# Kernel optimization log

Measured on AMD Instinct MI355X. Metric: run time of the kernel, lower is better.

The kernel has to match this reference:

```python
import jax, jax.numpy as jnp
import numpy as np

N, E, H, NODE_IN, EDGE_DIM, L = 10000, 400000, 128, 6, 3, 4
LN_EPS = 1e-5


def _lin_init(key, fan_in, fan_out):
    return jax.random.normal(key, (fan_in, fan_out), dtype=jnp.float32) / np.sqrt(fan_in)


def setup_inputs() -> dict:
    key = jax.random.key(0)
    ks = jax.random.split(key, 24)
    x = jax.random.normal(ks[0], (N, NODE_IN), dtype=jnp.float32)
    edge_index = jax.random.randint(ks[1], (2, E), 0, N, dtype=jnp.int64)
    edge_attr = jax.random.normal(ks[2], (E, EDGE_DIM), dtype=jnp.float32)
    # encoder
    enc_w1 = _lin_init(ks[3], NODE_IN, H); enc_b1 = jnp.zeros((H,), jnp.float32)
    enc_w2 = _lin_init(ks[4], H, H); enc_b2 = jnp.zeros((H,), jnp.float32)
    # per-layer stacked params [L, ...]
    msg_w1 = jax.vmap(lambda k: _lin_init(k, 2 * H + EDGE_DIM, H))(jax.random.split(ks[5], L))
    msg_b1 = jnp.zeros((L, H), jnp.float32)
    msg_w2 = jax.vmap(lambda k: _lin_init(k, H, H))(jax.random.split(ks[6], L))
    msg_b2 = jnp.zeros((L, H), jnp.float32)
    upd_w1 = jax.vmap(lambda k: _lin_init(k, 2 * H, H))(jax.random.split(ks[7], L))
    upd_b1 = jnp.zeros((L, H), jnp.float32)
    upd_w2 = jax.vmap(lambda k: _lin_init(k, H, H))(jax.random.split(ks[8], L))
    upd_b2 = jnp.zeros((L, H), jnp.float32)
    ln_g = jnp.ones((L, H), jnp.float32)
    ln_b = jnp.zeros((L, H), jnp.float32)
    # decoder
    dec_w1 = _lin_init(ks[9], H, H); dec_b1 = jnp.zeros((H,), jnp.float32)
    dec_w2 = _lin_init(ks[10], H, 1); dec_b2 = jnp.zeros((1,), jnp.float32)
    return dict(x=x, edge_index=edge_index, edge_attr=edge_attr,
                enc_w1=enc_w1, enc_b1=enc_b1, enc_w2=enc_w2, enc_b2=enc_b2,
                msg_w1=msg_w1, msg_b1=msg_b1, msg_w2=msg_w2, msg_b2=msg_b2,
                upd_w1=upd_w1, upd_b1=upd_b1, upd_w2=upd_w2, upd_b2=upd_b2,
                ln_g=ln_g, ln_b=ln_b,
                dec_w1=dec_w1, dec_b1=dec_b1, dec_w2=dec_w2, dec_b2=dec_b2)


def _layernorm(h, g, b):
    mu = jnp.mean(h, axis=-1, keepdims=True)
    var = jnp.mean(jnp.square(h - mu), axis=-1, keepdims=True)
    return (h - mu) * jax.lax.rsqrt(var + LN_EPS) * g + b


def reference(x, edge_index, edge_attr,
              enc_w1, enc_b1, enc_w2, enc_b2,
              msg_w1, msg_b1, msg_w2, msg_b2,
              upd_w1, upd_b1, upd_w2, upd_b2,
              ln_g, ln_b,
              dec_w1, dec_b1, dec_w2, dec_b2):
    src, tgt = edge_index[0], edge_index[1]  # PyG default flow: message from x_j=src to x_i=tgt
    # in-degree counts for mean aggregation (zero-degree nodes -> 0 output, like scatter_mean)
    counts = jax.ops.segment_sum(jnp.ones((E,), jnp.float32), tgt, num_segments=N)
    inv_counts = (1.0 / jnp.maximum(counts, 1.0))[:, None]
    # encoder
    h = jax.nn.relu(x @ enc_w1 + enc_b1) @ enc_w2 + enc_b2  # [N, H]
    for l in range(L):
        x_i = h[tgt]  # [E, H] target features
        x_j = h[src]  # [E, H] source features
        m_in = jnp.concatenate([x_i, x_j, edge_attr], axis=-1)  # [E, 2H+edge_dim]
        m = jax.nn.relu(m_in @ msg_w1[l] + msg_b1[l]) @ msg_w2[l] + msg_b2[l]  # [E, H]
        agg = jax.ops.segment_sum(m, tgt, num_segments=N) * inv_counts  # [N, H] mean aggregate
        u_in = jnp.concatenate([h, agg], axis=-1)  # [N, 2H]
        u = jax.nn.relu(u_in @ upd_w1[l] + upd_b1[l]) @ upd_w2[l] + upd_b2[l]
        h = _layernorm(u + h, ln_g[l], ln_b[l])  # residual (in==out channels)
    # decoder
    return jax.nn.relu(h @ dec_w1 + dec_b1) @ dec_w2 + dec_b2  # [N, 1]
```

## Files before the change

kernel.cpp:

```cpp
#include <hip/hip_runtime.h>

#define NN 10000
#define NE 400000
#define HD 128
#define NIN 6
#define EDIM 3
#define NL 4
#define CAP 96
#define LN_EPS 1e-5f

typedef unsigned short u16;
using short8 = __attribute__((ext_vector_type(8))) short;
using f32x4 = __attribute__((ext_vector_type(4))) float;

__device__ __forceinline__ u16 f2bf(float x) {
    unsigned u = __float_as_uint(x);
    return (u16)((u + 0x7fff + ((u >> 16) & 1)) >> 16);
}
__device__ __forceinline__ float bf2f(u16 h) { return __uint_as_float(((unsigned)h) << 16); }
__device__ __forceinline__ void split2(float x, u16& hi, u16& lo) {
    hi = f2bf(x);
    lo = f2bf(x - bf2f(hi));
}
#define MFMA(a, b, c) __builtin_amdgcn_mfma_f32_16x16x32_bf16((a), (b), (c), 0, 0, 0)


__global__ __launch_bounds__(256) void k_prepfrag(
    const float* __restrict__ msg_w2, const float* __restrict__ msg_b2, const float* __restrict__ upd_w1,
    const float* __restrict__ upd_w2, const float* __restrict__ msg_w1, const float* __restrict__ dec_w1,
    const float* __restrict__ enc_w2, float* __restrict__ c2, int* __restrict__ cnt,
    u16* __restrict__ fG1, u16* __restrict__ fG2, u16* __restrict__ fPQ,
    u16* __restrict__ fDec, u16* __restrict__ fEnc) {
    int idx = blockIdx.x * 256 + threadIdx.x;
    if (idx < 65536) {
        int l = idx >> 14, rem = idx & 16383, i = rem >> 7, jj = rem & 127;
        const float* U1b = upd_w1 + (size_t)l * 2 * HD * HD + (size_t)HD * HD;
        const float* W2 = msg_w2 + (size_t)l * HD * HD + (size_t)i * HD;
        float acc = 0.f;
        for (int t = 0; t < HD; ++t) acc += W2[t] * U1b[(size_t)t * HD + jj];
        int ct = jj >> 4;
        int ks = 4 + (i >> 5);
        int lane = (((i & 31) >> 3) << 4) | (jj & 15);
        int j = i & 7;
        int g = (l << 12) | (ct << 9) | (ks << 6) | lane;
        fG1[(size_t)g * 8 + j] = f2bf(acc);
    } else if (idx < 66048) {
        int r = idx - 65536;
        int l = r >> 7, jj = r & 127;
        const float* U1b = upd_w1 + (size_t)l * 2 * HD * HD + (size_t)HD * HD;
        const float* b2 = msg_b2 + l * HD;
        float acc = 0.f;
        for (int t = 0; t < HD; ++t) acc += b2[t] * U1b[(size_t)t * HD + jj];
        c2[r] = acc;
    } else if (idx < 76048) {
        cnt[idx - 66048] = 0;
    } else if (idx < 84240) {
        int gl = idx - 76048;
        int l = gl >> 11, rem = gl & 2047;
        int ct = rem >> 8, ks = (rem >> 6) & 3, lane = rem & 63;
        int n = ct * 16 + (lane & 15), kb = ks * 32 + ((lane >> 4) << 3);
        int g = (l << 12) | (ct << 9) | (ks << 6) | lane;
        u16* dst = fG1 + (size_t)g * 8;
        const float* U = upd_w1 + (size_t)l * 256 * 128;
#pragma unroll
        for (int j = 0; j < 8; ++j) dst[j] = f2bf(U[(size_t)(kb + j) * 128 + n]);
    } else if (idx < 92432) {
        int gg = idx - 84240;
        int l = gg >> 11, r = gg & 2047;
        int ct = r >> 8, ks = (r >> 6) & 3, lane = r & 63;
        int n = ct * 16 + (lane & 15), kb = ks * 32 + ((lane >> 4) << 3);
        u16* dst = fG2 + (size_t)gg * 8;
        const float* W = upd_w2 + (size_t)l * 128 * 128;
#pragma unroll
        for (int j = 0; j < 8; ++j) dst[j] = f2bf(W[(size_t)(kb + j) * 128 + n]);
    } else if (idx < 108816) {
        int gg = idx - 92432;
        int li = gg >> 12, r = gg & 4095;
        int ct = r >> 8, ks = (r >> 6) & 3, lane = r & 63;
        int n = ct * 16 + (lane & 15), kb = ks * 32 + ((lane >> 4) << 3);
        u16* dst = fPQ + (size_t)gg * 8;
        const float* W = msg_w1 + (size_t)li * (2 * HD + EDIM) * HD;
#pragma unroll
        for (int j = 0; j < 8; ++j) {
            int k = kb + j;
            float v = (n < 128) ? W[(size_t)k * 128 + n] : W[(size_t)(128 + k) * 128 + (n - 128)];
            dst[j] = f2bf(v);
        }
    } else if (idx < 110864) {
        int r = idx - 108816;
        int ct = r >> 8, ks = (r >> 6) & 3, lane = r & 63;
        int n = ct * 16 + (lane & 15), kb = ks * 32 + ((lane >> 4) << 3);
        u16* dst = fDec + (size_t)r * 8;
#pragma unroll
        for (int j = 0; j < 8; ++j) dst[j] = f2bf(dec_w1[(size_t)(kb + j) * 128 + n]);
    } else if (idx < 112912) {
        int r = idx - 110864;
        int ct = r >> 8, ks = (r >> 6) & 3, lane = r & 63;
        int n = ct * 16 + (lane & 15), kb = ks * 32 + ((lane >> 4) << 3);
        u16* dst = fEnc + (size_t)r * 8;
#pragma unroll
        for (int j = 0; j < 8; ++j) dst[j] = f2bf(enc_w2[(size_t)(kb + j) * 128 + n]);
    }
}


__global__ __launch_bounds__(512) void k_scatenc(
    const int* __restrict__ srcp, const int* __restrict__ tgtp, const float* __restrict__ eattr,
    int* __restrict__ cnt, float4* __restrict__ sea,
    const float* __restrict__ x, const float* __restrict__ ew1, const float* __restrict__ eb1,
    const u16* __restrict__ fEnc, const float* __restrict__ eb2, const u16* __restrict__ fPQ0,
    const float* __restrict__ mb1, u16* __restrict__ h_hi, u16* __restrict__ h_lo,
    float* __restrict__ PQf, u16* __restrict__ Qb) {
    __shared__ u16 tHi[2048], tLo[2048];
    if (blockIdx.x >= 625) {
        int e = (blockIdx.x - 625) * 512 + threadIdx.x;
        if (e < NE) {
            int t = tgtp[e];
            int pos = atomicAdd(&cnt[t], 1);
            if (pos < CAP) {
                sea[t * CAP + pos] = make_float4(eattr[e * 3], eattr[e * 3 + 1], eattr[e * 3 + 2],
                                                 __uint_as_float((unsigned)srcp[e]));
            }
        }
        return;
    }
    int tid = threadIdx.x, w = tid >> 6, lane = tid & 63, q = lane >> 4, c = lane & 15;
    int band = blockIdx.x * 16;
    {
        int col = w * 16 + c;
        float wv[NIN];
#pragma unroll
        for (int k = 0; k < NIN; ++k) wv[k] = ew1[k * HD + col];
        float ebv = eb1[col];
#pragma unroll
        for (int reg = 0; reg < 4; ++reg) {
            int row = band + q * 4 + reg;
            float t = ebv;
#pragma unroll
            for (int k = 0; k < NIN; ++k) t += x[(size_t)row * NIN + k] * wv[k];
            t = fmaxf(t, 0.f);
            u16 hi, lo;
            split2(t, hi, lo);
            int r16 = q * 4 + reg;
            int a = r16 * 128 + (((col >> 3) ^ r16) << 3) + (col & 7);
            tHi[a] = hi;
            tLo[a] = lo;
        }
    }
    __syncthreads();
    short8 aH[4], aL[4];
#pragma unroll
    for (int ks = 0; ks < 4; ++ks) {
        int a = c * 128 + (((ks * 4 + q) ^ c) << 3);
        aH[ks] = *(const short8*)&tHi[a];
        aL[ks] = *(const short8*)&tLo[a];
    }
    f32x4 acc = {0, 0, 0, 0};
    {
        const u16* fb = fEnc + (size_t)w * 4 * 512 + lane * 8;
#pragma unroll
        for (int ks = 0; ks < 4; ++ks) {
            short8 b = *(const short8*)(fb + ks * 512);
            acc = MFMA(aH[ks], b, acc);
            acc = MFMA(aL[ks], b, acc);
        }
    }
    __syncthreads();
    {
        int col = w * 16 + c;
        float ebv = eb2[col];
#pragma unroll
        for (int reg = 0; reg < 4; ++reg) {
            int r16 = q * 4 + reg, row = band + r16;
            float hval = acc[reg] + ebv;
            u16 hi, lo;
            split2(hval, hi, lo);
            h_hi[(size_t)row * HD + col] = hi;
            h_lo[(size_t)row * HD + col] = lo;
            int a = r16 * 128 + (((col >> 3) ^ r16) << 3) + (col & 7);
            tHi[a] = hi;
            tLo[a] = lo;
        }
    }
    __syncthreads();
#pragma unroll
    for (int ks = 0; ks < 4; ++ks) {
        int a = c * 128 + (((ks * 4 + q) ^ c) << 3);
        aH[ks] = *(const short8*)&tHi[a];
        aL[ks] = *(const short8*)&tLo[a];
    }
#pragma unroll
    for (int i = 0; i < 2; ++i) {
        int ctg = w * 2 + i;
        const u16* fb = fPQ0 + (size_t)ctg * 4 * 512 + lane * 8;
        f32x4 a3 = {0, 0, 0, 0};
#pragma unroll
        for (int ks = 0; ks < 4; ++ks) {
            short8 b = *(const short8*)(fb + ks * 512);
            a3 = MFMA(aH[ks], b, a3);
            a3 = MFMA(aL[ks], b, a3);
        }
        int col = ctg * 16 + c;
        if (ctg < 8) {
            float bias = mb1[col];
#pragma unroll
            for (int reg = 0; reg < 4; ++reg)
                PQf[(size_t)(band + q * 4 + reg) * HD + col] = a3[reg] + bias;
        } else {
            int colq = col - 128;
#pragma unroll
            for (int reg = 0; reg < 4; ++reg)
                Qb[(size_t)(band + q * 4 + reg) * HD + colq] = f2bf(a3[reg]);
        }
    }
}


template <bool LAST>
__global__ __launch_bounds__(512) void k_layer(
    const float* __restrict__ PQf_in, const u16* __restrict__ Qb_in,
    const int* __restrict__ cnt, const float4* __restrict__ sea, const float* __restrict__ wc,
    u16* __restrict__ h_hi, u16* __restrict__ h_lo,
    const u16* __restrict__ fG1, const u16* __restrict__ fG2,
    const float* __restrict__ ub1, const float* __restrict__ c2l, const float* __restrict__ ub2,
    const float* __restrict__ g, const float* __restrict__ bb,
    const u16* __restrict__ fPQ, const float* __restrict__ nb1,
    float* __restrict__ PQf_out, u16* __restrict__ Qb_out,
    const u16* __restrict__ fDec, const float* __restrict__ db1, const float* __restrict__ dw2,
    const float* __restrict__ db2, float* __restrict__ out) {
    __shared__ u16 sHi[2048], sLo[2048];
    __shared__ u16 tHi[2048], tLo[2048];
    __shared__ float red[16][8][2];
    int tid = threadIdx.x, w = tid >> 6, lane = tid & 63, q = lane >> 4, c = lane & 15;
    int band = blockIdx.x * 16;
    int j = lane * 2;
    {
        float2 wcr0 = *(const float2*)(wc + j);
        float2 wcr1 = *(const float2*)(wc + HD + j);
        float2 wcr2 = *(const float2*)(wc + 2 * HD + j);
#pragma unroll
        for (int i = 0; i < 2; ++i) {
            int r16 = w * 2 + i;
            int n = __builtin_amdgcn_readfirstlane(band + r16);
            int cn = cnt[n];
            float invn = 1.0f / fmaxf((float)cn, 1.0f);
            int cle = __builtin_amdgcn_readfirstlane(cn < CAP ? cn : CAP);
            float2 p = *(const float2*)(PQf_in + (size_t)n * HD + j);
            float acc0 = 0.f, acc1 = 0.f;
            const float4* bucket = sea + (size_t)n * CAP;
            auto edge1 = [&](float4 A) {
                int sv = (int)__float_as_uint(A.w);
                float c0 = A.x * wcr0.x + A.y * wcr1.x + A.z * wcr2.x;
                float c1 = A.x * wcr0.y + A.y * wcr1.y + A.z * wcr2.y;
                unsigned u = *(const unsigned*)(Qb_in + (size_t)sv * HD + j);
                acc0 += fmaxf(p.x + __uint_as_float(u << 16) + c0, 0.f);
                acc1 += fmaxf(p.y + __uint_as_float(u & 0xffff0000u) + c1, 0.f);
            };
            int e = 0;
            for (; e + 3 < cle; e += 4) {
                float4 A0 = bucket[e], A1 = bucket[e + 1], A2 = bucket[e + 2], A3 = bucket[e + 3];
                edge1(A0);
                edge1(A1);
                edge1(A2);
                edge1(A3);
            }
            for (; e < cle; ++e) edge1(bucket[e]);
            float v0 = acc0 * invn, v1 = acc1 * invn;
            u16 h0, l0, h1, l1;
            split2(v0, h0, l0);
            split2(v1, h1, l1);
            int a = r16 * 128 + (((j >> 3) ^ r16) << 3) + (j & 7);
            *(ushort2*)&sHi[a] = make_ushort2(h0, h1);
            *(ushort2*)&sLo[a] = make_ushort2(l0, l1);
        }
    }
    __syncthreads();
    short8 aH[8], aL[8];
    {
        size_t rb = (size_t)(band + c) * HD + q * 8;
#pragma unroll
        for (int ks = 0; ks < 4; ++ks) {
            aH[ks] = *(const short8*)(h_hi + rb + ks * 32);
            aL[ks] = *(const short8*)(h_lo + rb + ks * 32);
            int a = c * 128 + (((ks * 4 + q) ^ c) << 3);
            aH[4 + ks] = *(const short8*)&sHi[a];
            aL[4 + ks] = *(const short8*)&sLo[a];
        }
    }
    f32x4 acc = {0, 0, 0, 0};
    {
        const u16* fb = fG1 + (size_t)w * 8 * 512 + lane * 8;
#pragma unroll
        for (int ks = 0; ks < 8; ++ks) {
            short8 b = *(const short8*)(fb + ks * 512);
            acc = MFMA(aH[ks], b, acc);
            acc = MFMA(aL[ks], b, acc);
        }
    }
    float alv[4];
#pragma unroll
    for (int reg = 0; reg < 4; ++reg) alv[reg] = (cnt[band + q * 4 + reg] > 0) ? 1.f : 0.f;
    {
        int col = w * 16 + c;
        float u1b = ub1[col], cc = c2l[col];
#pragma unroll
        for (int reg = 0; reg < 4; ++reg) {
            int r16 = q * 4 + reg;
            float t = fmaxf(acc[reg] + u1b + alv[reg] * cc, 0.f);
            u16 hi, lo;
            split2(t, hi, lo);
            int a = r16 * 128 + (((col >> 3) ^ r16) << 3) + (col & 7);
            tHi[a] = hi;
            tLo[a] = lo;
        }
    }
    __syncthreads();
    short8 aH2[4], aL2[4];
#pragma unroll
    for (int ks = 0; ks < 4; ++ks) {
        int a = c * 128 + (((ks * 4 + q) ^ c) << 3);
        aH2[ks] = *(const short8*)&tHi[a];
        aL2[ks] = *(const short8*)&tLo[a];
    }
    f32x4 acc2 = {0, 0, 0, 0};
    {
        const u16* fb = fG2 + (size_t)w * 4 * 512 + lane * 8;
#pragma unroll
        for (int ks = 0; ks < 4; ++ks) {
            short8 b = *(const short8*)(fb + ks * 512);
            acc2 = MFMA(aH2[ks], b, acc2);
            acc2 = MFMA(aL2[ks], b, acc2);
        }
    }
    float vv[4];
    {
        int col = w * 16 + c;
        float u2b = ub2[col];
#pragma unroll
        for (int reg = 0; reg < 4; ++reg) {
            size_t idx = (size_t)(band + q * 4 + reg) * HD + col;
            float hres = bf2f(h_hi[idx]) + bf2f(h_lo[idx]);
            vv[reg] = acc2[reg] + u2b + hres;
        }
    }
#pragma unroll
    for (int reg = 0; reg < 4; ++reg) {
        float s = vv[reg];
        float s2 = vv[reg] * vv[reg];
        for (int m = 1; m < 16; m <<= 1) {
            s += __shfl_xor(s, m);
            s2 += __shfl_xor(s2, m);
        }
        if (c == 0) {
            red[q * 4 + reg][w][0] = s;
            red[q * 4 + reg][w][1] = s2;
        }
    }
    __syncthreads();
    float mu[4], rs[4];
#pragma unroll
    for (int reg = 0; reg < 4; ++reg) {
        int r16 = q * 4 + reg;
        float S1 = 0.f, S2 = 0.f;
#pragma unroll
        for (int ww = 0; ww < 8; ++ww) {
            S1 += red[r16][ww][0];
            S2 += red[r16][ww][1];
        }
        float m = S1 * (1.f / HD);
        float var = S2 * (1.f / HD) - m * m;
        mu[reg] = m;
        rs[reg] = rsqrtf(var + LN_EPS);
    }
    {
        int col = w * 16 + c;
        float gg = g[col], bv = bb[col];
#pragma unroll
        for (int reg = 0; reg < 4; ++reg) {
            int r16 = q * 4 + reg;
            float o = (vv[reg] - mu[reg]) * rs[reg] * gg + bv;
            u16 hi, lo;
            split2(o, hi, lo);
            int a = r16 * 128 + (((col >> 3) ^ r16) << 3) + (col & 7);
            tHi[a] = hi;
            tLo[a] = lo;
            if (!LAST) {
                size_t idx = (size_t)(band + r16) * HD + col;
                h_hi[idx] = hi;
                h_lo[idx] = lo;
            }
        }
    }
    __syncthreads();
    short8 aH3[4], aL3[4];
#pragma unroll
    for (int ks = 0; ks < 4; ++ks) {
        int a = c * 128 + (((ks * 4 + q) ^ c) << 3);
        aH3[ks] = *(const short8*)&tHi[a];
        aL3[ks] = *(const short8*)&tLo[a];
    }
    if (!LAST) {
#pragma unroll
        for (int i = 0; i < 2; ++i) {
            int ctg = w * 2 + i;
            const u16* fb = fPQ + (size_t)ctg * 4 * 512 + lane * 8;
            f32x4 a3 = {0, 0, 0, 0};
#pragma unroll
            for (int ks = 0; ks < 4; ++ks) {
                short8 b = *(const short8*)(fb + ks * 512);
                a3 = MFMA(aH3[ks], b, a3);
                a3 = MFMA(aL3[ks], b, a3);
            }
            int col = ctg * 16 + c;
            if (ctg < 8) {
                float bias = nb1[col];
#pragma unroll
                for (int reg = 0; reg < 4; ++reg)
                    PQf_out[(size_t)(band + q * 4 + reg) * HD + col] = a3[reg] + bias;
            } else {
                int colq = col - 128;
#pragma unroll
                for (int reg = 0; reg < 4; ++reg)
                    Qb_out[(size_t)(band + q * 4 + reg) * HD + colq] = f2bf(a3[reg]);
            }
        }
    } else {
        float part[4];
        {
            const u16* fb = fDec + (size_t)w * 4 * 512 + lane * 8;
            f32x4 a3 = {0, 0, 0, 0};
#pragma unroll
            for (int ks = 0; ks < 4; ++ks) {
                short8 b = *(const short8*)(fb + ks * 512);
                a3 = MFMA(aH3[ks], b, a3);
                a3 = MFMA(aL3[ks], b, a3);
            }
            int col = w * 16 + c;
            float w2v = dw2[col], b1v = db1[col];
#pragma unroll
            for (int reg = 0; reg < 4; ++reg) part[reg] = fmaxf(a3[reg] + b1v, 0.f) * w2v;
        }
#pragma unroll
        for (int reg = 0; reg < 4; ++reg) {
            float s = part[reg];
            for (int m = 1; m < 16; m <<= 1) s += __shfl_xor(s, m);
            if (c == 0) red[q * 4 + reg][w][0] = s;
        }
        __syncthreads();
        if (tid < 16) {
            float s = db2[0];
#pragma unroll
            for (int ww = 0; ww < 8; ++ww) s += red[tid][ww][0];
            out[band + tid] = s;
        }
    }
}


extern "C" void kernel_launch(void* const* d_in, const int* in_sizes, int n_in,
                              void* d_out, int out_size, void* d_ws, size_t ws_size,
                              hipStream_t stream) {
    const float* x = (const float*)d_in[0];
    const int* eidx = (const int*)d_in[1];
    const float* eattr = (const float*)d_in[2];
    const float* enc_w1 = (const float*)d_in[3];
    const float* enc_b1 = (const float*)d_in[4];
    const float* enc_w2 = (const float*)d_in[5];
    const float* enc_b2 = (const float*)d_in[6];
    const float* msg_w1 = (const float*)d_in[7];
    const float* msg_b1 = (const float*)d_in[8];
    const float* msg_w2 = (const float*)d_in[9];
    const float* msg_b2 = (const float*)d_in[10];
    const float* upd_w1 = (const float*)d_in[11];
    const float* upd_b1 = (const float*)d_in[12];
    const float* upd_w2 = (const float*)d_in[13];
    const float* upd_b2 = (const float*)d_in[14];
    const float* ln_g = (const float*)d_in[15];
    const float* ln_b = (const float*)d_in[16];
    const float* dec_w1 = (const float*)d_in[17];
    const float* dec_b1 = (const float*)d_in[18];
    const float* dec_w2 = (const float*)d_in[19];
    const float* dec_b2 = (const float*)d_in[20];
    const int* srcp = eidx;
    const int* tgtp = eidx + NE;

    char* base = (char*)d_ws;
    size_t off = 0;
    auto alloc = [&](size_t bytes) -> void* {
        off = (off + 15) & ~(size_t)15;
        void* p = base + off;
        off += bytes;
        return p;
    };
    float4* sea = (float4*)alloc((size_t)NN * CAP * 16);
    float* PQf0 = (float*)alloc((size_t)NN * HD * 4);
    float* PQf1 = (float*)alloc((size_t)NN * HD * 4);
    u16* Qb0 = (u16*)alloc((size_t)NN * HD * 2);
    u16* Qb1 = (u16*)alloc((size_t)NN * HD * 2);
    u16* h_hi = (u16*)alloc((size_t)NN * HD * 2);
    u16* h_lo = (u16*)alloc((size_t)NN * HD * 2);
    int* cnt = (int*)alloc((size_t)NN * 4);
    float* c2 = (float*)alloc((size_t)NL * HD * 4);
    u16* fG1 = (u16*)alloc((size_t)131072 * 2);
    u16* fG2 = (u16*)alloc((size_t)65536 * 2);
    u16* fPQ = (u16*)alloc((size_t)131072 * 2);
    u16* fDec = (u16*)alloc((size_t)16384 * 2);
    u16* fEnc = (u16*)alloc((size_t)16384 * 2);

    k_prepfrag<<<442, 256, 0, stream>>>(msg_w2, msg_b2, upd_w1, upd_w2, msg_w1, dec_w1, enc_w2,
                                        c2, cnt, fG1, fG2, fPQ, fDec, fEnc);
    k_scatenc<<<625 + (NE + 511) / 512, 512, 0, stream>>>(srcp, tgtp, eattr, cnt, sea,
                                                          x, enc_w1, enc_b1, fEnc, enc_b2, fPQ,
                                                          msg_b1, h_hi, h_lo, PQf0, Qb0);

    float* PQin = PQf0;
    u16* Qin = Qb0;
    float* PQout = PQf1;
    u16* Qout = Qb1;
    for (int l = 0; l < NL; ++l) {
        const float* wc = msg_w1 + (size_t)l * (2 * HD + EDIM) * HD + (size_t)2 * HD * HD;
        if (l < NL - 1) {
            k_layer<false><<<NN / 16, 512, 0, stream>>>(
                PQin, Qin, cnt, sea, wc, h_hi, h_lo,
                fG1 + (size_t)l * 32768, fG2 + (size_t)l * 16384,
                upd_b1 + l * HD, c2 + l * HD, upd_b2 + l * HD, ln_g + l * HD, ln_b + l * HD,
                fPQ + (size_t)(l + 1) * 32768, msg_b1 + (size_t)(l + 1) * HD, PQout, Qout,
                nullptr, nullptr, nullptr, nullptr, nullptr);
        } else {
            k_layer<true><<<NN / 16, 512, 0, stream>>>(
                PQin, Qin, cnt, sea, wc, h_hi, h_lo,
                fG1 + (size_t)l * 32768, fG2 + (size_t)l * 16384,
                upd_b1 + l * HD, c2 + l * HD, upd_b2 + l * HD, ln_g + l * HD, ln_b + l * HD,
                nullptr, nullptr, nullptr, nullptr,
                fDec, dec_b1, dec_w2, dec_b2, (float*)d_out);
        }
        float* tf = PQin; PQin = PQout; PQout = tf;
        u16* tq = Qin; Qin = Qout; Qout = tq;
    }
}
```

Measured before the change: 276.1 us.

## Move edge scatter into prep kernel and software-pipeline edge gather loop

The edge bucketing scatter moves out of the encoder kernel into the weight-fragment prep kernel, with the count reset replaced by a memset, so the scatter runs alongside weight preparation and the encoder launches as a smaller grid. In the layer kernel, the per-node edge loop is rewritten as a three-stage rotating pipeline: bucket entries are loaded two groups ahead and the dependent Q gathers one group ahead of the compute. This is meant to hide the two-level gather latency, at the cost of more registers and more complex tail handling.

```diff
diff --git a/kernel.cpp b/kernel.cpp
--- a/kernel.cpp
+++ b/kernel.cpp
@@ -25,12 +25,26 @@
 #define MFMA(a, b, c) __builtin_amdgcn_mfma_f32_16x16x32_bf16((a), (b), (c), 0, 0, 0)
 
 
-__global__ __launch_bounds__(256) void k_prepfrag(
+__global__ __launch_bounds__(256) void k_prepscat(
     const float* __restrict__ msg_w2, const float* __restrict__ msg_b2, const float* __restrict__ upd_w1,
     const float* __restrict__ upd_w2, const float* __restrict__ msg_w1, const float* __restrict__ dec_w1,
-    const float* __restrict__ enc_w2, float* __restrict__ c2, int* __restrict__ cnt,
+    const float* __restrict__ enc_w2, float* __restrict__ c2,
     u16* __restrict__ fG1, u16* __restrict__ fG2, u16* __restrict__ fPQ,
-    u16* __restrict__ fDec, u16* __restrict__ fEnc) {
+    u16* __restrict__ fDec, u16* __restrict__ fEnc,
+    const int* __restrict__ srcp, const int* __restrict__ tgtp, const float* __restrict__ eattr,
+    int* __restrict__ cnt, float4* __restrict__ sea) {
+    if (blockIdx.x >= 442) {
+        int e = (blockIdx.x - 442) * 256 + threadIdx.x;
+        if (e < NE) {
+            int t = tgtp[e];
+            int pos = atomicAdd(&cnt[t], 1);
+            if (pos < CAP) {
+                sea[t * CAP + pos] = make_float4(eattr[e * 3], eattr[e * 3 + 1], eattr[e * 3 + 2],
+                                                 __uint_as_float((unsigned)srcp[e]));
+            }
+        }
+        return;
+    }
     int idx = blockIdx.x * 256 + threadIdx.x;
     if (idx < 65536) {
         int l = idx >> 14, rem = idx & 16383, i = rem >> 7, jj = rem & 127;
@@ -53,7 +67,6 @@
         for (int t = 0; t < HD; ++t) acc += b2[t] * U1b[(size_t)t * HD + jj];
         c2[r] = acc;
     } else if (idx < 76048) {
-        cnt[idx - 66048] = 0;
     } else if (idx < 84240) {
         int gl = idx - 76048;
         int l = gl >> 11, rem = gl & 2047;
@@ -104,26 +117,12 @@
 }
 
 
-__global__ __launch_bounds__(512) void k_scatenc(
-    const int* __restrict__ srcp, const int* __restrict__ tgtp, const float* __restrict__ eattr,
-    int* __restrict__ cnt, float4* __restrict__ sea,
+__global__ __launch_bounds__(512) void k_enc(
     const float* __restrict__ x, const float* __restrict__ ew1, const float* __restrict__ eb1,
     const u16* __restrict__ fEnc, const float* __restrict__ eb2, const u16* __restrict__ fPQ0,
     const float* __restrict__ mb1, u16* __restrict__ h_hi, u16* __restrict__ h_lo,
     float* __restrict__ PQf, u16* __restrict__ Qb) {
     __shared__ u16 tHi[2048], tLo[2048];
-    if (blockIdx.x >= 625) {
-        int e = (blockIdx.x - 625) * 512 + threadIdx.x;
-        if (e < NE) {
-            int t = tgtp[e];
-            int pos = atomicAdd(&cnt[t], 1);
-            if (pos < CAP) {
-                sea[t * CAP + pos] = make_float4(eattr[e * 3], eattr[e * 3 + 1], eattr[e * 3 + 2],
-                                                 __uint_as_float((unsigned)srcp[e]));
-            }
-        }
-        return;
-    }
     int tid = threadIdx.x, w = tid >> 6, lane = tid & 63, q = lane >> 4, c = lane & 15;
     int band = blockIdx.x * 16;
     {
@@ -248,23 +247,61 @@
             float2 p = *(const float2*)(PQf_in + (size_t)n * HD + j);
             float acc0 = 0.f, acc1 = 0.f;
             const float4* bucket = sea + (size_t)n * CAP;
-            auto edge1 = [&](float4 A) {
-                int sv = (int)__float_as_uint(A.w);
+
+            float4 Aa[2], Ab[2], Ac[2];
+            unsigned Ua[2], Ub[2], Uc[2];
+            auto LA = [&](float4* A, int gg) {
+                A[0] = bucket[gg * 2];
+                A[1] = bucket[gg * 2 + 1];
+            };
+            auto IU = [&](const float4* A, unsigned* U) {
+                U[0] = *(const unsigned*)(Qb_in + (size_t)__float_as_uint(A[0].w) * HD + j);
+                U[1] = *(const unsigned*)(Qb_in + (size_t)__float_as_uint(A[1].w) * HD + j);
+            };
+            auto CO = [&](const float4* A, const unsigned* U) {
+#pragma unroll
+                for (int k = 0; k < 2; ++k) {
+                    float c0 = A[k].x * wcr0.x + A[k].y * wcr1.x + A[k].z * wcr2.x;
+                    float c1 = A[k].x * wcr0.y + A[k].y * wcr1.y + A[k].z * wcr2.y;
+                    unsigned u = U[k];
+                    acc0 += fmaxf(p.x + __uint_as_float(u << 16) + c0, 0.f);
+                    acc1 += fmaxf(p.y + __uint_as_float(u & 0xffff0000u) + c1, 0.f);
+                }
+            };
+
+            int ngrp = cle >> 1;
+            if (ngrp >= 2) {
+                LA(Aa, 0);
+                LA(Ab, 1);
+                IU(Aa, Ua);
+                int gi = 0;
+                for (; gi + 5 <= ngrp; gi += 3) {
+                    LA(Ac, gi + 2); IU(Ab, Ub); CO(Aa, Ua);
+                    LA(Aa, gi + 3); IU(Ac, Uc); CO(Ab, Ub);
+                    LA(Ab, gi + 4); IU(Aa, Ua); CO(Ac, Uc);
+                }
+                int r = ngrp - gi;
+                if (r == 2) {
+                    IU(Ab, Ub); CO(Aa, Ua); CO(Ab, Ub);
+                } else if (r == 3) {
+                    LA(Ac, gi + 2); IU(Ab, Ub); CO(Aa, Ua);
+                    IU(Ac, Uc); CO(Ab, Ub); CO(Ac, Uc);
+                } else {
+                    LA(Ac, gi + 2); IU(Ab, Ub); CO(Aa, Ua);
+                    LA(Aa, gi + 3); IU(Ac, Uc); CO(Ab, Ub);
+                    IU(Aa, Ua); CO(Ac, Uc); CO(Aa, Ua);
+                }
+            } else if (ngrp == 1) {
+                LA(Aa, 0); IU(Aa, Ua); CO(Aa, Ua);
+            }
+            if (cle & 1) {
+                float4 A = bucket[cle - 1];
+                unsigned u = *(const unsigned*)(Qb_in + (size_t)__float_as_uint(A.w) * HD + j);
                 float c0 = A.x * wcr0.x + A.y * wcr1.x + A.z * wcr2.x;
                 float c1 = A.x * wcr0.y + A.y * wcr1.y + A.z * wcr2.y;
-                unsigned u = *(const unsigned*)(Qb_in + (size_t)sv * HD + j);
                 acc0 += fmaxf(p.x + __uint_as_float(u << 16) + c0, 0.f);
                 acc1 += fmaxf(p.y + __uint_as_float(u & 0xffff0000u) + c1, 0.f);
-            };
-            int e = 0;
-            for (; e + 3 < cle; e += 4) {
-                float4 A0 = bucket[e], A1 = bucket[e + 1], A2 = bucket[e + 2], A3 = bucket[e + 3];
-                edge1(A0);
-                edge1(A1);
-                edge1(A2);
-                edge1(A3);
-            }
-            for (; e < cle; ++e) edge1(bucket[e]);
+            }
             float v0 = acc0 * invn, v1 = acc1 * invn;
             u16 h0, l0, h1, l1;
             split2(v0, h0, l0);
@@ -507,11 +544,13 @@
     u16* fDec = (u16*)alloc((size_t)16384 * 2);
     u16* fEnc = (u16*)alloc((size_t)16384 * 2);
 
-    k_prepfrag<<<442, 256, 0, stream>>>(msg_w2, msg_b2, upd_w1, upd_w2, msg_w1, dec_w1, enc_w2,
-                                        c2, cnt, fG1, fG2, fPQ, fDec, fEnc);
-    k_scatenc<<<625 + (NE + 511) / 512, 512, 0, stream>>>(srcp, tgtp, eattr, cnt, sea,
-                                                          x, enc_w1, enc_b1, fEnc, enc_b2, fPQ,
-                                                          msg_b1, h_hi, h_lo, PQf0, Qb0);
+    hipMemsetAsync(cnt, 0, (size_t)NN * 4, stream);
+    k_prepscat<<<442 + (NE + 255) / 256, 256, 0, stream>>>(
+        msg_w2, msg_b2, upd_w1, upd_w2, msg_w1, dec_w1, enc_w2,
+        c2, fG1, fG2, fPQ, fDec, fEnc,
+        srcp, tgtp, eattr, cnt, sea);
+    k_enc<<<625, 512, 0, stream>>>(x, enc_w1, enc_b1, fEnc, enc_b2, fPQ,
+                                   msg_b1, h_hi, h_lo, PQf0, Qb0);
 
     float* PQin = PQf0;
     u16* Qin = Qb0;
```

Result: slower. 302.9 us (+9.7%).

## Split per-node edge gather into separate chunked kernel with atomic accumulation

Applied to the files above, without the earlier changes.

Moves the per-node edge message gather out of the fused layer kernel into a new kernel where each node's edge bucket is split across six wavefronts. Each wavefront loads up to 16 edges with all loads issued up front and atomically adds its partial sums into a per-layer float buffer. The intent is more parallelism and memory-level concurrency for the gather-bound phase. It also moves the scatter into the weight-prep kernel, separates the encoder, and zeroes counts and sums with memsets. The cost is extra launches, a large zeroed scratch buffer, float atomics with nondeterministic summation order, and an extra round trip of the aggregate through global memory.

```diff
diff --git a/kernel.cpp b/kernel.cpp
--- a/kernel.cpp
+++ b/kernel.cpp
@@ -7,6 +7,7 @@
 #define EDIM 3
 #define NL 4
 #define CAP 96
+#define NCH 6
 #define LN_EPS 1e-5f
 
 typedef unsigned short u16;
@@ -25,12 +26,26 @@
 #define MFMA(a, b, c) __builtin_amdgcn_mfma_f32_16x16x32_bf16((a), (b), (c), 0, 0, 0)
 
 
-__global__ __launch_bounds__(256) void k_prepfrag(
+__global__ __launch_bounds__(256) void k_prepscat(
     const float* __restrict__ msg_w2, const float* __restrict__ msg_b2, const float* __restrict__ upd_w1,
     const float* __restrict__ upd_w2, const float* __restrict__ msg_w1, const float* __restrict__ dec_w1,
-    const float* __restrict__ enc_w2, float* __restrict__ c2, int* __restrict__ cnt,
+    const float* __restrict__ enc_w2, float* __restrict__ c2,
     u16* __restrict__ fG1, u16* __restrict__ fG2, u16* __restrict__ fPQ,
-    u16* __restrict__ fDec, u16* __restrict__ fEnc) {
+    u16* __restrict__ fDec, u16* __restrict__ fEnc,
+    const int* __restrict__ srcp, const int* __restrict__ tgtp, const float* __restrict__ eattr,
+    int* __restrict__ cnt, float4* __restrict__ sea) {
+    if (blockIdx.x >= 442) {
+        int e = (blockIdx.x - 442) * 256 + threadIdx.x;
+        if (e < NE) {
+            int t = tgtp[e];
+            int pos = atomicAdd(&cnt[t], 1);
+            if (pos < CAP) {
+                sea[t * CAP + pos] = make_float4(eattr[e * 3], eattr[e * 3 + 1], eattr[e * 3 + 2],
+                                                 __uint_as_float((unsigned)srcp[e]));
+            }
+        }
+        return;
+    }
     int idx = blockIdx.x * 256 + threadIdx.x;
     if (idx < 65536) {
         int l = idx >> 14, rem = idx & 16383, i = rem >> 7, jj = rem & 127;
@@ -53,7 +68,6 @@
         for (int t = 0; t < HD; ++t) acc += b2[t] * U1b[(size_t)t * HD + jj];
         c2[r] = acc;
     } else if (idx < 76048) {
-        cnt[idx - 66048] = 0;
     } else if (idx < 84240) {
         int gl = idx - 76048;
         int l = gl >> 11, rem = gl & 2047;
@@ -104,26 +118,12 @@
 }
 
 
-__global__ __launch_bounds__(512) void k_scatenc(
-    const int* __restrict__ srcp, const int* __restrict__ tgtp, const float* __restrict__ eattr,
-    int* __restrict__ cnt, float4* __restrict__ sea,
+__global__ __launch_bounds__(512) void k_enc(
     const float* __restrict__ x, const float* __restrict__ ew1, const float* __restrict__ eb1,
     const u16* __restrict__ fEnc, const float* __restrict__ eb2, const u16* __restrict__ fPQ0,
     const float* __restrict__ mb1, u16* __restrict__ h_hi, u16* __restrict__ h_lo,
     float* __restrict__ PQf, u16* __restrict__ Qb) {
     __shared__ u16 tHi[2048], tLo[2048];
-    if (blockIdx.x >= 625) {
-        int e = (blockIdx.x - 625) * 512 + threadIdx.x;
-        if (e < NE) {
-            int t = tgtp[e];
-            int pos = atomicAdd(&cnt[t], 1);
-            if (pos < CAP) {
-                sea[t * CAP + pos] = make_float4(eattr[e * 3], eattr[e * 3 + 1], eattr[e * 3 + 2],
-                                                 __uint_as_float((unsigned)srcp[e]));
-            }
-        }
-        return;
-    }
     int tid = threadIdx.x, w = tid >> 6, lane = tid & 63, q = lane >> 4, c = lane & 15;
     int band = blockIdx.x * 16;
     {
@@ -216,10 +216,50 @@
 }
 
 
+__global__ __launch_bounds__(256) void k_gath(
+    const float* __restrict__ PQf_in, const u16* __restrict__ Qb_in,
+    const int* __restrict__ cnt, const float4* __restrict__ sea,
+    const float* __restrict__ wc, float* __restrict__ S) {
+    int w = threadIdx.x >> 6, lane = threadIdx.x & 63;
+    int task = blockIdx.x * 4 + w;
+    int n = task / NCH;
+    int ch = task - n * NCH;
+    if (n >= NN) return;
+    int cn = cnt[n];
+    int cle = cn < CAP ? cn : CAP;
+    if (ch >= cle) return;
+    int nm = (cle - ch + (NCH - 1)) / NCH;
+    int j = lane * 2;
+    const float4* bk = sea + (size_t)n * CAP + ch;
+    float2 p = *(const float2*)(PQf_in + (size_t)n * HD + j);
+    float2 wcr0 = *(const float2*)(wc + j);
+    float2 wcr1 = *(const float2*)(wc + HD + j);
+    float2 wcr2 = *(const float2*)(wc + 2 * HD + j);
+    float4 A[16];
+    unsigned U[16];
+#pragma unroll
+    for (int k = 0; k < 16; ++k)
+        if (k < nm) A[k] = bk[k * NCH];
+#pragma unroll
+    for (int k = 0; k < 16; ++k)
+        if (k < nm) U[k] = *(const unsigned*)(Qb_in + (size_t)__float_as_uint(A[k].w) * HD + j);
+    float acc0 = 0.f, acc1 = 0.f;
+#pragma unroll
+    for (int k = 0; k < 16; ++k)
+        if (k < nm) {
+            float c0 = A[k].x * wcr0.x + A[k].y * wcr1.x + A[k].z * wcr2.x;
+            float c1 = A[k].x * wcr0.y + A[k].y * wcr1.y + A[k].z * wcr2.y;
+            acc0 += fmaxf(p.x + __uint_as_float(U[k] << 16) + c0, 0.f);
+            acc1 += fmaxf(p.y + __uint_as_float(U[k] & 0xffff0000u) + c1, 0.f);
+        }
+    atomicAdd(&S[(size_t)n * HD + j], acc0);
+    atomicAdd(&S[(size_t)n * HD + j + 1], acc1);
+}
+
+
 template <bool LAST>
 __global__ __launch_bounds__(512) void k_layer(
-    const float* __restrict__ PQf_in, const u16* __restrict__ Qb_in,
-    const int* __restrict__ cnt, const float4* __restrict__ sea, const float* __restrict__ wc,
+    const float* __restrict__ S, const int* __restrict__ cnt,
     u16* __restrict__ h_hi, u16* __restrict__ h_lo,
     const u16* __restrict__ fG1, const u16* __restrict__ fG2,
     const float* __restrict__ ub1, const float* __restrict__ c2l, const float* __restrict__ ub2,
@@ -235,37 +275,14 @@
     int band = blockIdx.x * 16;
     int j = lane * 2;
     {
-        float2 wcr0 = *(const float2*)(wc + j);
-        float2 wcr1 = *(const float2*)(wc + HD + j);
-        float2 wcr2 = *(const float2*)(wc + 2 * HD + j);
 #pragma unroll
         for (int i = 0; i < 2; ++i) {
             int r16 = w * 2 + i;
-            int n = __builtin_amdgcn_readfirstlane(band + r16);
+            int n = band + r16;
             int cn = cnt[n];
             float invn = 1.0f / fmaxf((float)cn, 1.0f);
-            int cle = __builtin_amdgcn_readfirstlane(cn < CAP ? cn : CAP);
-            float2 p = *(const float2*)(PQf_in + (size_t)n * HD + j);
-            float acc0 = 0.f, acc1 = 0.f;
-            const float4* bucket = sea + (size_t)n * CAP;
-            auto edge1 = [&](float4 A) {
-                int sv = (int)__float_as_uint(A.w);
-                float c0 = A.x * wcr0.x + A.y * wcr1.x + A.z * wcr2.x;
-                float c1 = A.x * wcr0.y + A.y * wcr1.y + A.z * wcr2.y;
-                unsigned u = *(const unsigned*)(Qb_in + (size_t)sv * HD + j);
-                acc0 += fmaxf(p.x + __uint_as_float(u << 16) + c0, 0.f);
-                acc1 += fmaxf(p.y + __uint_as_float(u & 0xffff0000u) + c1, 0.f);
-            };
-            int e = 0;
-            for (; e + 3 < cle; e += 4) {
-                float4 A0 = bucket[e], A1 = bucket[e + 1], A2 = bucket[e + 2], A3 = bucket[e + 3];
-                edge1(A0);
-                edge1(A1);
-                edge1(A2);
-                edge1(A3);
-            }
-            for (; e < cle; ++e) edge1(bucket[e]);
-            float v0 = acc0 * invn, v1 = acc1 * invn;
+            float2 s = *(const float2*)(S + (size_t)n * HD + j);
+            float v0 = s.x * invn, v1 = s.y * invn;
             u16 h0, l0, h1, l1;
             split2(v0, h0, l0);
             split2(v1, h1, l1);
@@ -506,29 +523,36 @@
     u16* fPQ = (u16*)alloc((size_t)131072 * 2);
     u16* fDec = (u16*)alloc((size_t)16384 * 2);
     u16* fEnc = (u16*)alloc((size_t)16384 * 2);
-
-    k_prepfrag<<<442, 256, 0, stream>>>(msg_w2, msg_b2, upd_w1, upd_w2, msg_w1, dec_w1, enc_w2,
-                                        c2, cnt, fG1, fG2, fPQ, fDec, fEnc);
-    k_scatenc<<<625 + (NE + 511) / 512, 512, 0, stream>>>(srcp, tgtp, eattr, cnt, sea,
-                                                          x, enc_w1, enc_b1, fEnc, enc_b2, fPQ,
-                                                          msg_b1, h_hi, h_lo, PQf0, Qb0);
+    float* Sbuf = (float*)alloc((size_t)NL * NN * HD * 4);
+
+    hipMemsetAsync(cnt, 0, (size_t)NN * 4, stream);
+    hipMemsetAsync(Sbuf, 0, (size_t)NL * NN * HD * 4, stream);
+    k_prepscat<<<442 + (NE + 255) / 256, 256, 0, stream>>>(
+        msg_w2, msg_b2, upd_w1, upd_w2, msg_w1, dec_w1, enc_w2,
+        c2, fG1, fG2, fPQ, fDec, fEnc,
+        srcp, tgtp, eattr, cnt, sea);
+    k_enc<<<625, 512, 0, stream>>>(x, enc_w1, enc_b1, fEnc, enc_b2, fPQ,
+                                   msg_b1, h_hi, h_lo, PQf0, Qb0);
 
     float* PQin = PQf0;
     u16* Qin = Qb0;
     float* PQout = PQf1;
     u16* Qout = Qb1;
+    const int gath_blocks = (NN * NCH + 3) / 4;
     for (int l = 0; l < NL; ++l) {
         const float* wc = msg_w1 + (size_t)l * (2 * HD + EDIM) * HD + (size_t)2 * HD * HD;
+        float* Sl = Sbuf + (size_t)l * NN * HD;
+        k_gath<<<gath_blocks, 256, 0, stream>>>(PQin, Qin, cnt, sea, wc, Sl);
         if (l < NL - 1) {
             k_layer<false><<<NN / 16, 512, 0, stream>>>(
-                PQin, Qin, cnt, sea, wc, h_hi, h_lo,
+                Sl, cnt, h_hi, h_lo,
                 fG1 + (size_t)l * 32768, fG2 + (size_t)l * 16384,
                 upd_b1 + l * HD, c2 + l * HD, upd_b2 + l * HD, ln_g + l * HD, ln_b + l * HD,
                 fPQ + (size_t)(l + 1) * 32768, msg_b1 + (size_t)(l + 1) * HD, PQout, Qout,
                 nullptr, nullptr, nullptr, nullptr, nullptr);
         } else {
             k_layer<true><<<NN / 16, 512, 0, stream>>>(
-                PQin, Qin, cnt, sea, wc, h_hi, h_lo,
+                Sl, cnt, h_hi, h_lo,
                 fG1 + (size_t)l * 32768, fG2 + (size_t)l * 16384,
                 upd_b1 + l * HD, c2 + l * HD, upd_b2 + l * HD, ln_g + l * HD, ln_b + l * HD,
                 nullptr, nullptr, nullptr, nullptr,
```

Result: slower. 509.4 us (+84.5%).
